# Kernel optimization log

Hardware: AMD Instinct MI355X
Metric: run time of the kernel (lower is better)

The kernel has to match this reference:

```python
import jax, jax.numpy as jnp
import numpy as np

N_NODES = 100000   # number of nodes
N_EDGES = 20000    # number of hyperedges
N_INC = 800000     # incidence (node, hyperedge) pairs
TEXT_DIM = 384     # all-MiniLM-L6-v2 sentence embedding dim
HID = 128          # hidden_dim in _init_model


def setup_inputs() -> dict:
    key = jax.random.key(0)
    ks = jax.random.split(key, 16)
    s = 1.0 / np.sqrt(HID)
    inp = {
        "text_emb": jax.random.normal(ks[0], (N_NODES, TEXT_DIM), jnp.float32),
        "W_proj": jax.random.normal(ks[1], (TEXT_DIM, HID), jnp.float32) / np.sqrt(TEXT_DIM),
        "b_proj": jnp.zeros((HID,), jnp.float32),
        # weight generator 0 (Linear-ReLU-Dropout(eval)-Linear)
        "W1a": jax.random.normal(ks[2], (HID, HID), jnp.float32) * s,
        "b1a": jnp.zeros((HID,), jnp.float32),
        "W2a": jax.random.normal(ks[3], (HID, HID), jnp.float32) * s,
        "b2a": jnp.zeros((HID,), jnp.float32),
        # weight generator 1
        "W1b": jax.random.normal(ks[4], (HID, HID), jnp.float32) * s,
        "b1b": jnp.zeros((HID,), jnp.float32),
        "W2b": jax.random.normal(ks[5], (HID, HID), jnp.float32) * s,
        "b2b": jnp.zeros((HID,), jnp.float32),
        "node_idx": jax.random.randint(ks[6], (N_INC,), 0, N_NODES),
        "edge_idx": jax.random.randint(ks[7], (N_INC,), 0, N_EDGES),
    }
    return inp


def _segment_mean(vals, idx, num_segments):
    # vals: [E_inc, D]; idx: [E_inc] -> [num_segments, D]
    ssum = jax.ops.segment_sum(vals, idx, num_segments=num_segments)
    cnt = jax.ops.segment_sum(jnp.ones((idx.shape[0], 1), vals.dtype), idx,
                              num_segments=num_segments)
    return ssum / jnp.maximum(cnt, 1.0)


def reference(text_emb, W_proj, b_proj,
              W1a, b1a, W2a, b2a,
              W1b, b1b, W2b, b2b,
              node_idx, edge_idx):
    # text projection to hidden space: [N, 128]
    h = text_emb @ W_proj + b_proj
    gens = ((W1a, b1a, W2a, b2a), (W1b, b1b, W2b, b2b))
    for (W1, b1, W2, b2) in gens:  # 2 hypergraph layers (fixed by code)
        # hypernetwork: generate per-layer dynamic modulation from pooled context
        g = jnp.mean(h, axis=0)                               # [128]
        scale = jnp.maximum(g @ W1 + b1, 0.0) @ W2 + b2       # [128]
        # gather node -> hyperedge, aggregate (mean) per hyperedge
        e_feat = _segment_mean(h[node_idx], edge_idx, N_EDGES)   # [E, 128]
        # gather hyperedge -> node, aggregate (mean) per node (scatter)
        m = _segment_mean(e_feat[edge_idx], node_idx, N_NODES)   # [N, 128]
        h = jax.nn.relu(m * scale)
    return h
```

## Files before the change

kernel.cpp:

```cpp
#include <hip/hip_runtime.h>

#define N_NODES 100000
#define N_EDGES 20000
#define N_INC   800000
#define TDIM    384
#define HID     128
#define NOFF    800000
#define NKEYS   120000
#define EPAD    8
#define NPAD    4

#define WPREP_BLOCKS 24
#define CNT_BLOCKS   1024
#define PROJ_BLOCKS  1563
#define FILL_BLOCKS  3125
#define SCAN_BLOCKS  118
#define EAGG_BLOCKS  5000
#define NAGG_BLOCKS  2500

typedef __attribute__((ext_vector_type(8))) short short8;
typedef __attribute__((ext_vector_type(4))) float floatx4;

static __device__ __forceinline__ unsigned short f32_bf16_rne(float f) {
  unsigned int u = __float_as_uint(f);
  unsigned int r = u + 0x7FFFu + ((u >> 16) & 1u);
  return (unsigned short)(r >> 16);
}

__global__ __launch_bounds__(256) void prep_count_kernel(
    const float* __restrict__ W, unsigned short* __restrict__ Bh,
    unsigned short* __restrict__ Bl,
    const int* __restrict__ node_idx, const int* __restrict__ edge_idx,
    int* __restrict__ ecp, int* __restrict__ ncp,
    int* __restrict__ rank_e, int* __restrict__ rank_n)
{
  const int tid = threadIdx.x;
  if (blockIdx.x < WPREP_BLOCKS) {
    int b = blockIdx.x * 4 + (tid >> 6);
    int lane = tid & 63;
    int kk = b >> 3, nt = b & 7;
    int col = lane & 15, quad = lane >> 4;
    size_t o = ((size_t)b * 64 + lane) * 8;
#pragma unroll
    for (int j = 0; j < 8; ++j) {
      int k = kk * 32 + quad * 8 + j;
      float w = W[(size_t)k * HID + nt * 16 + col];
      unsigned short h = f32_bf16_rne(w);
      float hf = __uint_as_float((unsigned int)h << 16);
      Bh[o + j] = h;
      Bl[o + j] = f32_bf16_rne(w - hf);
    }
    return;
  }
  int start = (blockIdx.x - WPREP_BLOCKS) * 256 + tid;
  for (int i = start; i < N_INC; i += CNT_BLOCKS * 256) {
    int ed = edge_idx[i];
    int nd = node_idx[i];
    rank_e[i] = atomicAdd(&ecp[ed * EPAD], 1);
    rank_n[i] = atomicAdd(&ncp[nd * NPAD], 1);
  }
}

static __device__ __forceinline__ int padded_cnt(const int* ecp, const int* ncp, int i) {
  return (i < N_EDGES) ? ecp[i * EPAD] : ncp[(i - N_EDGES) * NPAD];
}

__global__ __launch_bounds__(1024) void scan_lookback(
    const int* __restrict__ ecp, const int* __restrict__ ncp,
    int* __restrict__ ptr, unsigned* __restrict__ status, int n)
{
  __shared__ int s[1024];
  __shared__ int carry_s;
  const int tid = threadIdx.x;
  const int b = blockIdx.x;
  int i = b * 1024 + tid;
  int v = (i < n) ? padded_cnt(ecp, ncp, i) : 0;
  s[tid] = v;
  __syncthreads();
  for (int off = 1; off < 1024; off <<= 1) {
    int add = (tid >= off) ? s[tid - off] : 0;
    __syncthreads();
    s[tid] += add;
    __syncthreads();
  }
  int incl = s[tid];
  int agg = s[1023];
  if (tid == 0) {
    unsigned pack = (b == 0) ? ((2u << 30) | (unsigned)agg)
                             : ((1u << 30) | (unsigned)agg);
    __hip_atomic_store(&status[b], pack, __ATOMIC_RELEASE, __HIP_MEMORY_SCOPE_AGENT);
  }
  int carry = 0;
  if (b > 0) {
    if (tid == 0) {
      int pb = b - 1;
      for (;;) {
        unsigned st = __hip_atomic_load(&status[pb], __ATOMIC_ACQUIRE,
                                        __HIP_MEMORY_SCOPE_AGENT);
        unsigned state = st >> 30;
        if (state == 0u) continue;
        carry += (int)(st & 0x3FFFFFFFu);
        if (state == 2u) break;
        --pb;
      }
      __hip_atomic_store(&status[b], (2u << 30) | (unsigned)(carry + agg),
                         __ATOMIC_RELEASE, __HIP_MEMORY_SCOPE_AGENT);
      carry_s = carry;
    }
    __syncthreads();
    carry = carry_s;
  }
  if (i < n) ptr[i] = carry + incl - v;
  if (b == SCAN_BLOCKS - 1 && tid == 1023) ptr[n] = carry + incl;
}

__global__ __launch_bounds__(256) void proj_fill_kernel(
    const float* __restrict__ A, const unsigned short* __restrict__ Bh,
    const unsigned short* __restrict__ Bl, const float* __restrict__ bias,
    unsigned short* __restrict__ Hb, float* __restrict__ gsum0,
    const int* __restrict__ node_idx, const int* __restrict__ edge_idx,
    const int* __restrict__ rank_e, const int* __restrict__ rank_n,
    const int* __restrict__ eptr, const int* __restrict__ nptr,
    int* __restrict__ ecols, int* __restrict__ ncols)
{
  __shared__ unsigned short BhS[512 * 8];
  __shared__ unsigned short BlS[512 * 8];
  __shared__ float red[4][HID];
  const int tid = threadIdx.x;

  if (blockIdx.x >= PROJ_BLOCKS) {
    int i = (blockIdx.x - PROJ_BLOCKS) * 256 + tid;
    int ed = edge_idx[i];
    int nd = node_idx[i];
    int p = eptr[ed] + rank_e[i];
    int q = nptr[nd] - NOFF + rank_n[i];
    __builtin_nontemporal_store(nd, &ecols[p]);
    __builtin_nontemporal_store(ed, &ncols[q]);
    return;
  }

  const int wave = tid >> 6;
  const int lane = tid & 63;
  const int col = lane & 15;
  const int quad = lane >> 4;
  const int m0 = blockIdx.x * 64 + wave * 16;

  floatx4 acc[8];
#pragma unroll
  for (int nt = 0; nt < 8; ++nt) acc[nt] = (floatx4){0.f, 0.f, 0.f, 0.f};

  int r = m0 + col;
  if (r >= N_NODES) r = N_NODES - 1;
  const float* arow = A + (size_t)r * TDIM + quad * 8;

  float ra[8];
  *(float4*)(&ra[0]) = *(const float4*)(arow);
  *(float4*)(&ra[4]) = *(const float4*)(arow + 4);

  for (int kk = 0; kk < 12; ++kk) {
    short8 sh0 = *(const short8*)(Bh + ((size_t)kk * 512 + tid) * 8);
    short8 sh1 = *(const short8*)(Bh + ((size_t)kk * 512 + tid + 256) * 8);
    short8 sl0 = *(const short8*)(Bl + ((size_t)kk * 512 + tid) * 8);
    short8 sl1 = *(const short8*)(Bl + ((size_t)kk * 512 + tid + 256) * 8);
    __syncthreads();
    *(short8*)(BhS + (size_t)tid * 8) = sh0;
    *(short8*)(BhS + ((size_t)tid + 256) * 8) = sh1;
    *(short8*)(BlS + (size_t)tid * 8) = sl0;
    *(short8*)(BlS + ((size_t)tid + 256) * 8) = sl1;

    float rn[8];
    if (kk < 11) {
      *(float4*)(&rn[0]) = *(const float4*)(arow + (kk + 1) * 32);
      *(float4*)(&rn[4]) = *(const float4*)(arow + (kk + 1) * 32 + 4);
    }

    short8 ah, al;
#pragma unroll
    for (int j = 0; j < 8; ++j) {
      float f = ra[j];
      unsigned short h = f32_bf16_rne(f);
      float hf = __uint_as_float((unsigned int)h << 16);
      ah[j] = (short)h;
      al[j] = (short)f32_bf16_rne(f - hf);
    }
    __syncthreads();

#pragma unroll
    for (int nt = 0; nt < 8; ++nt) {
      short8 bh = *(const short8*)(BhS + ((size_t)nt * 64 + lane) * 8);
      short8 bl = *(const short8*)(BlS + ((size_t)nt * 64 + lane) * 8);
      acc[nt] = __builtin_amdgcn_mfma_f32_16x16x32_bf16(ah, bh, acc[nt], 0, 0, 0);
      acc[nt] = __builtin_amdgcn_mfma_f32_16x16x32_bf16(al, bh, acc[nt], 0, 0, 0);
      acc[nt] = __builtin_amdgcn_mfma_f32_16x16x32_bf16(ah, bl, acc[nt], 0, 0, 0);
    }
#pragma unroll
    for (int j = 0; j < 8; ++j) ra[j] = rn[j];
  }

#pragma unroll
  for (int nt = 0; nt < 8; ++nt) {
    float bv = bias[nt * 16 + col];
    float p = 0.f;
#pragma unroll
    for (int rr = 0; rr < 4; ++rr) {
      int row = m0 + quad * 4 + rr;
      float v = acc[nt][rr] + bv;
      if (row < N_NODES) {
        Hb[(size_t)row * HID + nt * 16 + col] = f32_bf16_rne(v);
        p += v;
      }
    }
    p += __shfl_xor(p, 16, 64);
    p += __shfl_xor(p, 32, 64);
    if (quad == 0) red[wave][nt * 16 + col] = p;
  }
  __syncthreads();
  if (tid < HID) {
    float a = red[0][tid] + red[1][tid] + red[2][tid] + red[3][tid];
    atomicAdd(&gsum0[(blockIdx.x & 7) * HID + tid], a);
  }
}

__global__ __launch_bounds__(256) void edge_agg_scale_kernel(
    const unsigned short* __restrict__ Hb, const int* __restrict__ eptr,
    const int* __restrict__ ecols, unsigned short* __restrict__ Eb,
    const float* __restrict__ gsum,
    const float* __restrict__ W1, const float* __restrict__ b1,
    const float* __restrict__ W2, const float* __restrict__ b2,
    float* __restrict__ scale)
{
  if (blockIdx.x >= EAGG_BLOCKS) {
    __shared__ float g[HID], t[HID];
    int c = threadIdx.x;
    if (c < HID) {
      float s = 0.f;
#pragma unroll
      for (int k = 0; k < 8; ++k) s += gsum[k * HID + c];
      g[c] = s * (1.0f / (float)N_NODES);
    }
    __syncthreads();
    if (c < HID) {
      float acc = b1[c];
#pragma unroll 8
      for (int k = 0; k < HID; ++k) acc += g[k] * W1[(size_t)k * HID + c];
      t[c] = fmaxf(acc, 0.f);
    }
    __syncthreads();
    if (c < HID) {
      float acc2 = b2[c];
#pragma unroll 8
      for (int k = 0; k < HID; ++k) acc2 += t[k] * W2[(size_t)k * HID + c];
      scale[c] = acc2;
    }
    return;
  }
  int gw = blockIdx.x * 4 + (threadIdx.x >> 6);
  int lane = threadIdx.x & 63;
  int p0 = eptr[gw], p1 = eptr[gw + 1];
  float ax0 = 0.f, ay0 = 0.f, ax1 = 0.f, ay1 = 0.f;
  float ax2 = 0.f, ay2 = 0.f, ax3 = 0.f, ay3 = 0.f;
  for (int base = p0; base < p1; base += 64) {
    int cnt = min(64, p1 - base);
    int idx = (base + lane < p1) ? ecols[base + lane] : 0;
    int j = 0;
    for (; j + 3 < cnt; j += 4) {
      int n0 = __shfl(idx, j, 64);
      int n1 = __shfl(idx, j + 1, 64);
      int n2 = __shfl(idx, j + 2, 64);
      int n3 = __shfl(idx, j + 3, 64);
      unsigned v0 = *(const unsigned*)(Hb + (size_t)n0 * HID + lane * 2);
      unsigned v1 = *(const unsigned*)(Hb + (size_t)n1 * HID + lane * 2);
      unsigned v2 = *(const unsigned*)(Hb + (size_t)n2 * HID + lane * 2);
      unsigned v3 = *(const unsigned*)(Hb + (size_t)n3 * HID + lane * 2);
      ax0 += __uint_as_float(v0 << 16); ay0 += __uint_as_float(v0 & 0xffff0000u);
      ax1 += __uint_as_float(v1 << 16); ay1 += __uint_as_float(v1 & 0xffff0000u);
      ax2 += __uint_as_float(v2 << 16); ay2 += __uint_as_float(v2 & 0xffff0000u);
      ax3 += __uint_as_float(v3 << 16); ay3 += __uint_as_float(v3 & 0xffff0000u);
    }
    for (; j < cnt; ++j) {
      int n0 = __shfl(idx, j, 64);
      unsigned v0 = *(const unsigned*)(Hb + (size_t)n0 * HID + lane * 2);
      ax0 += __uint_as_float(v0 << 16); ay0 += __uint_as_float(v0 & 0xffff0000u);
    }
  }
  float inv = 1.f / (float)max(p1 - p0, 1);
  float sx = ((ax0 + ax1) + (ax2 + ax3)) * inv;
  float sy = ((ay0 + ay1) + (ay2 + ay3)) * inv;
  unsigned pk = ((unsigned)f32_bf16_rne(sy) << 16) | f32_bf16_rne(sx);
  *(unsigned*)(Eb + (size_t)gw * HID + lane * 2) = pk;
}

__global__ __launch_bounds__(256) void node_agg_kernel(
    const unsigned short* __restrict__ Eb, const int* __restrict__ nptr,
    const int* __restrict__ ncols, const float* __restrict__ scale,
    unsigned short* __restrict__ Hb, float* __restrict__ H,
    float* __restrict__ gsum, int do_aux)
{
  __shared__ float red[4][HID];
  int wave = threadIdx.x >> 6, lane = threadIdx.x & 63;
  float2 sc = *(const float2*)(scale + lane * 2);
  float csx = 0.f, csy = 0.f;
  for (int gw = blockIdx.x * 4 + wave; gw < N_NODES; gw += NAGG_BLOCKS * 4) {
    int p0 = nptr[gw] - NOFF, p1 = nptr[gw + 1] - NOFF;
    float ax0 = 0.f, ay0 = 0.f, ax1 = 0.f, ay1 = 0.f;
    float ax2 = 0.f, ay2 = 0.f, ax3 = 0.f, ay3 = 0.f;
    for (int base = p0; base < p1; base += 64) {
      int cnt = min(64, p1 - base);
      int idx = (base + lane < p1) ? ncols[base + lane] : 0;
      int j = 0;
      for (; j + 3 < cnt; j += 4) {
        int e0 = __shfl(idx, j, 64);
        int e1 = __shfl(idx, j + 1, 64);
        int e2 = __shfl(idx, j + 2, 64);
        int e3 = __shfl(idx, j + 3, 64);
        unsigned v0 = *(const unsigned*)(Eb + (size_t)e0 * HID + lane * 2);
        unsigned v1 = *(const unsigned*)(Eb + (size_t)e1 * HID + lane * 2);
        unsigned v2 = *(const unsigned*)(Eb + (size_t)e2 * HID + lane * 2);
        unsigned v3 = *(const unsigned*)(Eb + (size_t)e3 * HID + lane * 2);
        ax0 += __uint_as_float(v0 << 16); ay0 += __uint_as_float(v0 & 0xffff0000u);
        ax1 += __uint_as_float(v1 << 16); ay1 += __uint_as_float(v1 & 0xffff0000u);
        ax2 += __uint_as_float(v2 << 16); ay2 += __uint_as_float(v2 & 0xffff0000u);
        ax3 += __uint_as_float(v3 << 16); ay3 += __uint_as_float(v3 & 0xffff0000u);
      }
      for (; j < cnt; ++j) {
        int e0 = __shfl(idx, j, 64);
        unsigned v0 = *(const unsigned*)(Eb + (size_t)e0 * HID + lane * 2);
        ax0 += __uint_as_float(v0 << 16); ay0 += __uint_as_float(v0 & 0xffff0000u);
      }
    }
    float inv = 1.f / (float)max(p1 - p0, 1);
    float ox = fmaxf(((ax0 + ax1) + (ax2 + ax3)) * inv * sc.x, 0.f);
    float oy = fmaxf(((ay0 + ay1) + (ay2 + ay3)) * inv * sc.y, 0.f);
    if (do_aux) {
      unsigned pk = ((unsigned)f32_bf16_rne(oy) << 16) | f32_bf16_rne(ox);
      *(unsigned*)(Hb + (size_t)gw * HID + lane * 2) = pk;
      csx += ox; csy += oy;
    } else {
      *(float2*)(H + (size_t)gw * HID + lane * 2) = make_float2(ox, oy);
    }
  }
  if (do_aux) {
    red[wave][lane * 2] = csx;
    red[wave][lane * 2 + 1] = csy;
    __syncthreads();
    if (threadIdx.x < HID) {
      int c = threadIdx.x;
      float a = red[0][c] + red[1][c] + red[2][c] + red[3][c];
      atomicAdd(&gsum[(blockIdx.x & 7) * HID + c], a);
    }
  }
}

extern "C" void kernel_launch(void* const* d_in, const int* in_sizes, int n_in,
                              void* d_out, int out_size, void* d_ws, size_t ws_size,
                              hipStream_t stream)
{
  const float* text = (const float*)d_in[0];
  const float* Wp   = (const float*)d_in[1];
  const float* bp   = (const float*)d_in[2];
  const float* W1a  = (const float*)d_in[3];
  const float* b1a  = (const float*)d_in[4];
  const float* W2a  = (const float*)d_in[5];
  const float* b2a  = (const float*)d_in[6];
  const float* W1b  = (const float*)d_in[7];
  const float* b1b  = (const float*)d_in[8];
  const float* W2b  = (const float*)d_in[9];
  const float* b2b  = (const float*)d_in[10];
  const int* node_idx = (const int*)d_in[11];
  const int* edge_idx = (const int*)d_in[12];
  float* H = (float*)d_out;

  char* ws = (char*)d_ws;
  int*      ecp    = (int*)(ws + 0);
  int*      ncp    = (int*)(ws + 640000);
  float*    gsum0  = (float*)(ws + 2240000);
  float*    gsum1  = (float*)(ws + 2244096);
  unsigned* status = (unsigned*)(ws + 2248192);
  const size_t zero_bytes = 2248704;
  int*   cptr  = (int*)(ws + 2248704);
  int*   eptr  = cptr;
  int*   nptr  = cptr + N_EDGES;
  int*   ecols = (int*)(ws + 2728712);
  int*   ncols = (int*)(ws + 5928712);
  float* scale0 = (float*)(ws + 9128712);
  float* scale1 = (float*)(ws + 9129224);
  unsigned short* Eb = (unsigned short*)(ws + 9130000);
  unsigned short* Hb = (unsigned short*)(ws + 14250000);
  int* rank_e = (int*)d_out;
  int* rank_n = rank_e + N_INC;
  unsigned short* Bh = (unsigned short*)((char*)d_out + 6400000);
  unsigned short* Bl = (unsigned short*)((char*)d_out + 6498304);

  hipMemsetAsync(ws, 0, zero_bytes, stream);

  prep_count_kernel<<<WPREP_BLOCKS + CNT_BLOCKS, 256, 0, stream>>>(
      Wp, Bh, Bl, node_idx, edge_idx, ecp, ncp, rank_e, rank_n);

  scan_lookback<<<SCAN_BLOCKS, 1024, 0, stream>>>(ecp, ncp, cptr, status, NKEYS);

  proj_fill_kernel<<<PROJ_BLOCKS + FILL_BLOCKS, 256, 0, stream>>>(
      text, Bh, Bl, bp, Hb, gsum0, node_idx, edge_idx,
      rank_e, rank_n, eptr, nptr, ecols, ncols);

  edge_agg_scale_kernel<<<EAGG_BLOCKS + 1, 256, 0, stream>>>(
      Hb, eptr, ecols, Eb, gsum0, W1a, b1a, W2a, b2a, scale0);
  node_agg_kernel<<<NAGG_BLOCKS, 256, 0, stream>>>(
      Eb, nptr, ncols, scale0, Hb, H, gsum1, 1);

  edge_agg_scale_kernel<<<EAGG_BLOCKS + 1, 256, 0, stream>>>(
      Hb, eptr, ecols, Eb, gsum1, W1b, b1b, W2b, b2b, scale1);
  node_agg_kernel<<<NAGG_BLOCKS, 256, 0, stream>>>(
      Eb, nptr, ncols, scale1, Hb, H, gsum1, 0);
}
```

Measured before the change: 589.3 us.

## Reschedule CSR build: overlap projection with counting, node fill with edge aggregation

Moves the dense text projection GEMM into the same launch as the incidence counting atomics, so the counting blocks run alongside the MFMA work instead of alongside the fill. Weight prep becomes its own small kernel. The edge-CSR fill becomes a standalone kernel, and the node-CSR fill is folded into the first edge-aggregation launch as extra blocks, because node columns are only needed by the following node aggregation. This rebalances which independent work shares each launch to hide the latency-bound scatter phases, at the cost of one extra kernel launch and a larger first edge-aggregation grid.

```diff
diff --git a/kernel.cpp b/kernel.cpp
--- a/kernel.cpp
+++ b/kernel.cpp
@@ -10,13 +10,13 @@
 #define EPAD    8
 #define NPAD    4
 
-#define WPREP_BLOCKS 24
-#define CNT_BLOCKS   1024
-#define PROJ_BLOCKS  1563
-#define FILL_BLOCKS  3125
-#define SCAN_BLOCKS  118
-#define EAGG_BLOCKS  5000
-#define NAGG_BLOCKS  2500
+#define PROJ_BLOCKS 1563
+#define CNT_BLOCKS  512
+#define FILLE_BLOCKS 3125
+#define FILLN_BLOCKS 3125
+#define SCAN_BLOCKS 118
+#define EAGG_BLOCKS 5000
+#define NAGG_BLOCKS 2500
 
 typedef __attribute__((ext_vector_type(8))) short short8;
 typedef __attribute__((ext_vector_type(4))) float floatx4;
@@ -27,37 +27,129 @@
   return (unsigned short)(r >> 16);
 }
 
-__global__ __launch_bounds__(256) void prep_count_kernel(
+__global__ __launch_bounds__(64) void wprep_kernel(
     const float* __restrict__ W, unsigned short* __restrict__ Bh,
-    unsigned short* __restrict__ Bl,
+    unsigned short* __restrict__ Bl)
+{
+  int b = blockIdx.x;
+  int lane = threadIdx.x;
+  int kk = b >> 3, nt = b & 7;
+  int col = lane & 15, quad = lane >> 4;
+  size_t o = ((size_t)b * 64 + lane) * 8;
+#pragma unroll
+  for (int j = 0; j < 8; ++j) {
+    int k = kk * 32 + quad * 8 + j;
+    float w = W[(size_t)k * HID + nt * 16 + col];
+    unsigned short h = f32_bf16_rne(w);
+    float hf = __uint_as_float((unsigned int)h << 16);
+    Bh[o + j] = h;
+    Bl[o + j] = f32_bf16_rne(w - hf);
+  }
+}
+
+__global__ __launch_bounds__(256) void proj_count_kernel(
+    const float* __restrict__ A, const unsigned short* __restrict__ Bh,
+    const unsigned short* __restrict__ Bl, const float* __restrict__ bias,
+    unsigned short* __restrict__ Hb, float* __restrict__ gsum0,
     const int* __restrict__ node_idx, const int* __restrict__ edge_idx,
     int* __restrict__ ecp, int* __restrict__ ncp,
     int* __restrict__ rank_e, int* __restrict__ rank_n)
 {
+  __shared__ unsigned short BhS[512 * 8];
+  __shared__ unsigned short BlS[512 * 8];
+  __shared__ float red[4][HID];
   const int tid = threadIdx.x;
-  if (blockIdx.x < WPREP_BLOCKS) {
-    int b = blockIdx.x * 4 + (tid >> 6);
-    int lane = tid & 63;
-    int kk = b >> 3, nt = b & 7;
-    int col = lane & 15, quad = lane >> 4;
-    size_t o = ((size_t)b * 64 + lane) * 8;
+
+  if (blockIdx.x >= PROJ_BLOCKS) {
+    int start = (blockIdx.x - PROJ_BLOCKS) * 256 + tid;
+    for (int i = start; i < N_INC; i += CNT_BLOCKS * 256) {
+      int ed = edge_idx[i];
+      int nd = node_idx[i];
+      rank_e[i] = atomicAdd(&ecp[ed * EPAD], 1);
+      rank_n[i] = atomicAdd(&ncp[nd * NPAD], 1);
+    }
+    return;
+  }
+
+  const int wave = tid >> 6;
+  const int lane = tid & 63;
+  const int col = lane & 15;
+  const int quad = lane >> 4;
+  const int m0 = blockIdx.x * 64 + wave * 16;
+
+  floatx4 acc[8];
+#pragma unroll
+  for (int nt = 0; nt < 8; ++nt) acc[nt] = (floatx4){0.f, 0.f, 0.f, 0.f};
+
+  int r = m0 + col;
+  if (r >= N_NODES) r = N_NODES - 1;
+  const float* arow = A + (size_t)r * TDIM + quad * 8;
+
+  float ra[8];
+  *(float4*)(&ra[0]) = *(const float4*)(arow);
+  *(float4*)(&ra[4]) = *(const float4*)(arow + 4);
+
+  for (int kk = 0; kk < 12; ++kk) {
+    short8 sh0 = *(const short8*)(Bh + ((size_t)kk * 512 + tid) * 8);
+    short8 sh1 = *(const short8*)(Bh + ((size_t)kk * 512 + tid + 256) * 8);
+    short8 sl0 = *(const short8*)(Bl + ((size_t)kk * 512 + tid) * 8);
+    short8 sl1 = *(const short8*)(Bl + ((size_t)kk * 512 + tid + 256) * 8);
+    __syncthreads();
+    *(short8*)(BhS + (size_t)tid * 8) = sh0;
+    *(short8*)(BhS + ((size_t)tid + 256) * 8) = sh1;
+    *(short8*)(BlS + (size_t)tid * 8) = sl0;
+    *(short8*)(BlS + ((size_t)tid + 256) * 8) = sl1;
+
+    float rn[8];
+    if (kk < 11) {
+      *(float4*)(&rn[0]) = *(const float4*)(arow + (kk + 1) * 32);
+      *(float4*)(&rn[4]) = *(const float4*)(arow + (kk + 1) * 32 + 4);
+    }
+
+    short8 ah, al;
 #pragma unroll
     for (int j = 0; j < 8; ++j) {
-      int k = kk * 32 + quad * 8 + j;
-      float w = W[(size_t)k * HID + nt * 16 + col];
-      unsigned short h = f32_bf16_rne(w);
+      float f = ra[j];
+      unsigned short h = f32_bf16_rne(f);
       float hf = __uint_as_float((unsigned int)h << 16);
-      Bh[o + j] = h;
-      Bl[o + j] = f32_bf16_rne(w - hf);
-    }
-    return;
-  }
-  int start = (blockIdx.x - WPREP_BLOCKS) * 256 + tid;
-  for (int i = start; i < N_INC; i += CNT_BLOCKS * 256) {
-    int ed = edge_idx[i];
-    int nd = node_idx[i];
-    rank_e[i] = atomicAdd(&ecp[ed * EPAD], 1);
-    rank_n[i] = atomicAdd(&ncp[nd * NPAD], 1);
+      ah[j] = (short)h;
+      al[j] = (short)f32_bf16_rne(f - hf);
+    }
+    __syncthreads();
+
+#pragma unroll
+    for (int nt = 0; nt < 8; ++nt) {
+      short8 bh = *(const short8*)(BhS + ((size_t)nt * 64 + lane) * 8);
+      short8 bl = *(const short8*)(BlS + ((size_t)nt * 64 + lane) * 8);
+      acc[nt] = __builtin_amdgcn_mfma_f32_16x16x32_bf16(ah, bh, acc[nt], 0, 0, 0);
+      acc[nt] = __builtin_amdgcn_mfma_f32_16x16x32_bf16(al, bh, acc[nt], 0, 0, 0);
+      acc[nt] = __builtin_amdgcn_mfma_f32_16x16x32_bf16(ah, bl, acc[nt], 0, 0, 0);
+    }
+#pragma unroll
+    for (int j = 0; j < 8; ++j) ra[j] = rn[j];
+  }
+
+#pragma unroll
+  for (int nt = 0; nt < 8; ++nt) {
+    float bv = bias[nt * 16 + col];
+    float p = 0.f;
+#pragma unroll
+    for (int rr = 0; rr < 4; ++rr) {
+      int row = m0 + quad * 4 + rr;
+      float v = acc[nt][rr] + bv;
+      if (row < N_NODES) {
+        Hb[(size_t)row * HID + nt * 16 + col] = f32_bf16_rne(v);
+        p += v;
+      }
+    }
+    p += __shfl_xor(p, 16, 64);
+    p += __shfl_xor(p, 32, 64);
+    if (quad == 0) red[wave][nt * 16 + col] = p;
+  }
+  __syncthreads();
+  if (tid < HID) {
+    float a = red[0][tid] + red[1][tid] + red[2][tid] + red[3][tid];
+    atomicAdd(&gsum0[(blockIdx.x & 7) * HID + tid], a);
   }
 }
 
@@ -114,111 +206,16 @@
   if (b == SCAN_BLOCKS - 1 && tid == 1023) ptr[n] = carry + incl;
 }
 
-__global__ __launch_bounds__(256) void proj_fill_kernel(
-    const float* __restrict__ A, const unsigned short* __restrict__ Bh,
-    const unsigned short* __restrict__ Bl, const float* __restrict__ bias,
-    unsigned short* __restrict__ Hb, float* __restrict__ gsum0,
+__global__ __launch_bounds__(256) void fill_e_kernel(
     const int* __restrict__ node_idx, const int* __restrict__ edge_idx,
-    const int* __restrict__ rank_e, const int* __restrict__ rank_n,
-    const int* __restrict__ eptr, const int* __restrict__ nptr,
-    int* __restrict__ ecols, int* __restrict__ ncols)
-{
-  __shared__ unsigned short BhS[512 * 8];
-  __shared__ unsigned short BlS[512 * 8];
-  __shared__ float red[4][HID];
-  const int tid = threadIdx.x;
-
-  if (blockIdx.x >= PROJ_BLOCKS) {
-    int i = (blockIdx.x - PROJ_BLOCKS) * 256 + tid;
-    int ed = edge_idx[i];
-    int nd = node_idx[i];
-    int p = eptr[ed] + rank_e[i];
-    int q = nptr[nd] - NOFF + rank_n[i];
-    __builtin_nontemporal_store(nd, &ecols[p]);
-    __builtin_nontemporal_store(ed, &ncols[q]);
-    return;
-  }
-
-  const int wave = tid >> 6;
-  const int lane = tid & 63;
-  const int col = lane & 15;
-  const int quad = lane >> 4;
-  const int m0 = blockIdx.x * 64 + wave * 16;
-
-  floatx4 acc[8];
-#pragma unroll
-  for (int nt = 0; nt < 8; ++nt) acc[nt] = (floatx4){0.f, 0.f, 0.f, 0.f};
-
-  int r = m0 + col;
-  if (r >= N_NODES) r = N_NODES - 1;
-  const float* arow = A + (size_t)r * TDIM + quad * 8;
-
-  float ra[8];
-  *(float4*)(&ra[0]) = *(const float4*)(arow);
-  *(float4*)(&ra[4]) = *(const float4*)(arow + 4);
-
-  for (int kk = 0; kk < 12; ++kk) {
-    short8 sh0 = *(const short8*)(Bh + ((size_t)kk * 512 + tid) * 8);
-    short8 sh1 = *(const short8*)(Bh + ((size_t)kk * 512 + tid + 256) * 8);
-    short8 sl0 = *(const short8*)(Bl + ((size_t)kk * 512 + tid) * 8);
-    short8 sl1 = *(const short8*)(Bl + ((size_t)kk * 512 + tid + 256) * 8);
-    __syncthreads();
-    *(short8*)(BhS + (size_t)tid * 8) = sh0;
-    *(short8*)(BhS + ((size_t)tid + 256) * 8) = sh1;
-    *(short8*)(BlS + (size_t)tid * 8) = sl0;
-    *(short8*)(BlS + ((size_t)tid + 256) * 8) = sl1;
-
-    float rn[8];
-    if (kk < 11) {
-      *(float4*)(&rn[0]) = *(const float4*)(arow + (kk + 1) * 32);
-      *(float4*)(&rn[4]) = *(const float4*)(arow + (kk + 1) * 32 + 4);
-    }
-
-    short8 ah, al;
-#pragma unroll
-    for (int j = 0; j < 8; ++j) {
-      float f = ra[j];
-      unsigned short h = f32_bf16_rne(f);
-      float hf = __uint_as_float((unsigned int)h << 16);
-      ah[j] = (short)h;
-      al[j] = (short)f32_bf16_rne(f - hf);
-    }
-    __syncthreads();
-
-#pragma unroll
-    for (int nt = 0; nt < 8; ++nt) {
-      short8 bh = *(const short8*)(BhS + ((size_t)nt * 64 + lane) * 8);
-      short8 bl = *(const short8*)(BlS + ((size_t)nt * 64 + lane) * 8);
-      acc[nt] = __builtin_amdgcn_mfma_f32_16x16x32_bf16(ah, bh, acc[nt], 0, 0, 0);
-      acc[nt] = __builtin_amdgcn_mfma_f32_16x16x32_bf16(al, bh, acc[nt], 0, 0, 0);
-      acc[nt] = __builtin_amdgcn_mfma_f32_16x16x32_bf16(ah, bl, acc[nt], 0, 0, 0);
-    }
-#pragma unroll
-    for (int j = 0; j < 8; ++j) ra[j] = rn[j];
-  }
-
-#pragma unroll
-  for (int nt = 0; nt < 8; ++nt) {
-    float bv = bias[nt * 16 + col];
-    float p = 0.f;
-#pragma unroll
-    for (int rr = 0; rr < 4; ++rr) {
-      int row = m0 + quad * 4 + rr;
-      float v = acc[nt][rr] + bv;
-      if (row < N_NODES) {
-        Hb[(size_t)row * HID + nt * 16 + col] = f32_bf16_rne(v);
-        p += v;
-      }
-    }
-    p += __shfl_xor(p, 16, 64);
-    p += __shfl_xor(p, 32, 64);
-    if (quad == 0) red[wave][nt * 16 + col] = p;
-  }
-  __syncthreads();
-  if (tid < HID) {
-    float a = red[0][tid] + red[1][tid] + red[2][tid] + red[3][tid];
-    atomicAdd(&gsum0[(blockIdx.x & 7) * HID + tid], a);
-  }
+    const int* __restrict__ rank_e, const int* __restrict__ eptr,
+    int* __restrict__ ecols)
+{
+  int i = blockIdx.x * 256 + threadIdx.x;
+  int ed = edge_idx[i];
+  int nd = node_idx[i];
+  int p = eptr[ed] + rank_e[i];
+  __builtin_nontemporal_store(nd, &ecols[p]);
 }
 
 __global__ __launch_bounds__(256) void edge_agg_scale_kernel(
@@ -227,9 +224,20 @@
     const float* __restrict__ gsum,
     const float* __restrict__ W1, const float* __restrict__ b1,
     const float* __restrict__ W2, const float* __restrict__ b2,
-    float* __restrict__ scale)
-{
-  if (blockIdx.x >= EAGG_BLOCKS) {
+    float* __restrict__ scale,
+    const int* __restrict__ node_idx, const int* __restrict__ edge_idx,
+    const int* __restrict__ rank_n, const int* __restrict__ nptr,
+    int* __restrict__ ncols)
+{
+  if (blockIdx.x > EAGG_BLOCKS) {
+    int i = (blockIdx.x - EAGG_BLOCKS - 1) * 256 + threadIdx.x;
+    int ed = edge_idx[i];
+    int nd = node_idx[i];
+    int q = nptr[nd] - NOFF + rank_n[i];
+    __builtin_nontemporal_store(ed, &ncols[q]);
+    return;
+  }
+  if (blockIdx.x == EAGG_BLOCKS) {
     __shared__ float g[HID], t[HID];
     int c = threadIdx.x;
     if (c < HID) {
@@ -393,22 +401,24 @@
 
   hipMemsetAsync(ws, 0, zero_bytes, stream);
 
-  prep_count_kernel<<<WPREP_BLOCKS + CNT_BLOCKS, 256, 0, stream>>>(
-      Wp, Bh, Bl, node_idx, edge_idx, ecp, ncp, rank_e, rank_n);
+  wprep_kernel<<<96, 64, 0, stream>>>(Wp, Bh, Bl);
+  proj_count_kernel<<<PROJ_BLOCKS + CNT_BLOCKS, 256, 0, stream>>>(
+      text, Bh, Bl, bp, Hb, gsum0, node_idx, edge_idx, ecp, ncp, rank_e, rank_n);
 
   scan_lookback<<<SCAN_BLOCKS, 1024, 0, stream>>>(ecp, ncp, cptr, status, NKEYS);
 
-  proj_fill_kernel<<<PROJ_BLOCKS + FILL_BLOCKS, 256, 0, stream>>>(
-      text, Bh, Bl, bp, Hb, gsum0, node_idx, edge_idx,
-      rank_e, rank_n, eptr, nptr, ecols, ncols);
-
-  edge_agg_scale_kernel<<<EAGG_BLOCKS + 1, 256, 0, stream>>>(
-      Hb, eptr, ecols, Eb, gsum0, W1a, b1a, W2a, b2a, scale0);
+  fill_e_kernel<<<FILLE_BLOCKS, 256, 0, stream>>>(
+      node_idx, edge_idx, rank_e, eptr, ecols);
+
+  edge_agg_scale_kernel<<<EAGG_BLOCKS + 1 + FILLN_BLOCKS, 256, 0, stream>>>(
+      Hb, eptr, ecols, Eb, gsum0, W1a, b1a, W2a, b2a, scale0,
+      node_idx, edge_idx, rank_n, nptr, ncols);
   node_agg_kernel<<<NAGG_BLOCKS, 256, 0, stream>>>(
       Eb, nptr, ncols, scale0, Hb, H, gsum1, 1);
 
   edge_agg_scale_kernel<<<EAGG_BLOCKS + 1, 256, 0, stream>>>(
-      Hb, eptr, ecols, Eb, gsum1, W1b, b1b, W2b, b2b, scale1);
+      Hb, eptr, ecols, Eb, gsum1, W1b, b1b, W2b, b2b, scale1,
+      node_idx, edge_idx, rank_n, nptr, ncols);
   node_agg_kernel<<<NAGG_BLOCKS, 256, 0, stream>>>(
       Eb, nptr, ncols, scale1, Hb, H, gsum1, 0);
 }
```

Result: faster. 562.4 us (-4.6%).
